# Optimization experiments

Hardware: AMD Instinct MI355X
Metric: run time of the kernel (lower is better)

The kernel has to match this reference:

```python
import jax, jax.numpy as jnp
import numpy as np

V, DW, DH, OUT = 50000, 300, 50, 4
B, T = 1024, 200


def setup_inputs() -> dict:
    key = jax.random.key(0)
    ks = jax.random.split(key, 9)
    x = jax.random.randint(ks[0], (B, T), 0, V)
    lengs = jax.random.randint(ks[1], (B,), 1, T + 1)  # valid lengths >= 1
    k = 1.0 / np.sqrt(DH)
    emb = jax.random.normal(ks[2], (V, DW), jnp.float32)
    emb = emb.at[0].set(0.0)  # padding_idx=0
    w_ih = jax.random.uniform(ks[3], (4 * DH, DW), jnp.float32, -k, k)
    w_hh = jax.random.uniform(ks[4], (4 * DH, DH), jnp.float32, -k, k)
    b_ih = jax.random.uniform(ks[5], (4 * DH,), jnp.float32, -k, k)
    b_hh = jax.random.uniform(ks[6], (4 * DH,), jnp.float32, -k, k)
    w_out = jax.random.uniform(ks[7], (OUT, DH), jnp.float32, -k, k)
    b_out = jax.random.uniform(ks[8], (OUT,), jnp.float32, -k, k)
    return {"x": x, "lengs": lengs, "emb": emb, "w_ih": w_ih, "w_hh": w_hh,
            "b_ih": b_ih, "b_hh": b_hh, "w_out": w_out, "b_out": b_out}


def reference(x, lengs, emb, w_ih, w_hh, b_ih, b_hh, w_out, b_out):
    b, t = x.shape
    xe = emb[x]                                        # [B,T,DW]
    mask = jnp.arange(t)[None, :] < lengs[:, None]     # [B,T] valid steps
    bias = b_ih + b_hh                                 # [4*DH]

    def step(carry, inp):
        h, c = carry
        x_t, m_t = inp                                 # [B,DW], [B]
        g = x_t @ w_ih.T + h @ w_hh.T + bias           # [B,4*DH]
        i, f, gg, o = jnp.split(g, 4, axis=-1)         # torch gate order i,f,g,o
        c_new = jax.nn.sigmoid(f) * c + jax.nn.sigmoid(i) * jnp.tanh(gg)
        h_new = jax.nn.sigmoid(o) * jnp.tanh(c_new)
        m = m_t[:, None]
        # packed-sequence semantics: state frozen past each sequence's length
        return (jnp.where(m, h_new, h), jnp.where(m, c_new, c)), None

    h0 = jnp.zeros((b, DH), xe.dtype)
    (h, _), _ = jax.lax.scan(step, (h0, h0),
                             (xe.transpose(1, 0, 2), mask.T))
    logits = h @ w_out.T + b_out                       # hidden.view(B,-1) -> Linear
    return jax.nn.softmax(logits, axis=1)
```

## Files before the change

kernel.cpp:

```cpp
#include <hip/hip_runtime.h>
#include <math.h>

#define VOCAB 50000
#define DW 300
#define DH 50
#define G4 200
#define BATCH 1024
#define TMAX 200
#define OUTC 4

__global__ __launch_bounds__(256) void transpose_wih(
    const float* __restrict__ w_ih, float* __restrict__ w_T)
{
    int i = blockIdx.x * 256 + threadIdx.x;
    if (i < G4 * DW) {
        int u = i / DW, k = i % DW;
        w_T[k * G4 + u] = w_ih[i];
    }
}

__global__ __launch_bounds__(256, 2) void proj_kernel(
    const float* __restrict__ emb, const float* __restrict__ w_T,
    const float* __restrict__ b_ih, const float* __restrict__ b_hh,
    float* __restrict__ emb_proj)
{
    __shared__ __align__(16) float e_s[100 * 108];
    const int tid = threadIdx.x;
    const int v0 = blockIdx.x * 100;
    const int m_idx = tid / 25;
    const int n_idx = tid % 25;

    float acc[10][8];
#pragma unroll
    for (int m = 0; m < 10; m++)
#pragma unroll
        for (int c = 0; c < 8; c++) acc[m][c] = 0.f;

    for (int kc = 0; kc < DW; kc += 100) {
        __syncthreads();
        for (int i = tid; i < 2500; i += 256) {
            int r = i / 25, c = i % 25;
            float4 v = *(const float4*)&emb[(size_t)(v0 + r) * DW + kc + c * 4];
            *(float4*)&e_s[r * 108 + c * 4] = v;
        }
        __syncthreads();

        if (tid < 250) {
#pragma unroll 2
            for (int kk = 0; kk < 25; kk++) {
                float4 e4[10];
#pragma unroll
                for (int m = 0; m < 10; m++)
                    e4[m] = *(const float4*)&e_s[(m_idx * 10 + m) * 108 + kk * 4];
                const float* wbase = w_T + (size_t)(kc + kk * 4) * G4 + n_idx * 8;
#pragma unroll
                for (int j = 0; j < 4; j++) {
                    float4 wa = *(const float4*)(wbase + j * G4);
                    float4 wb = *(const float4*)(wbase + j * G4 + 4);
#pragma unroll
                    for (int m = 0; m < 10; m++) {
                        float ev = (j == 0) ? e4[m].x : (j == 1) ? e4[m].y
                                 : (j == 2) ? e4[m].z : e4[m].w;
                        acc[m][0] = fmaf(ev, wa.x, acc[m][0]);
                        acc[m][1] = fmaf(ev, wa.y, acc[m][1]);
                        acc[m][2] = fmaf(ev, wa.z, acc[m][2]);
                        acc[m][3] = fmaf(ev, wa.w, acc[m][3]);
                        acc[m][4] = fmaf(ev, wb.x, acc[m][4]);
                        acc[m][5] = fmaf(ev, wb.y, acc[m][5]);
                        acc[m][6] = fmaf(ev, wb.z, acc[m][6]);
                        acc[m][7] = fmaf(ev, wb.w, acc[m][7]);
                    }
                }
            }
        }
    }

    if (tid < 250) {
#pragma unroll
        for (int c = 0; c < 8; c++) {
            int u = n_idx * 8 + c;
            float bias = b_ih[u] + b_hh[u];
            int u2 = (u % DH) * 4 + (u / DH);
#pragma unroll
            for (int m = 0; m < 10; m++)
                emb_proj[(size_t)(v0 + m_idx * 10 + m) * G4 + u2] = acc[m][c] + bias;
        }
    }
}

__device__ __forceinline__ float tanh_f(float x) {
    float e2 = __expf(fminf(2.f * x, 60.f));
    return (e2 - 1.f) / (e2 + 1.f);
}

__global__ __launch_bounds__(64, 1) void lstm_kernel(
    const int* __restrict__ x, const int* __restrict__ lengs,
    const float* __restrict__ emb_proj, const float* __restrict__ w_hh,
    const float* __restrict__ w_out, const float* __restrict__ b_out,
    float* __restrict__ out)
{
    __shared__ __align__(16) float h_s[52];
    __shared__ int x_s[TMAX];
    __shared__ float red[OUTC];

    const int l  = threadIdx.x;
    const int b  = blockIdx.x;
    const int ll = (l < DH) ? l : DH - 1;
    const int len = lengs[b];

    for (int i = l; i < TMAX; i += 64) x_s[i] = x[b * TMAX + i];
    if (l < 52) h_s[l] = 0.f;

    float4 rwi[13], rwf[13], rwg[13], rwo[13];
    {
        const float* wr;
#define LOADROW(dst, gate)                                                    \
        wr = w_hh + (size_t)((gate) * DH + ll) * DH;                          \
        _Pragma("unroll")                                                     \
        for (int k4 = 0; k4 < 12; k4++) {                                     \
            float2 a = *(const float2*)(wr + 4 * k4);                         \
            float2 bb = *(const float2*)(wr + 4 * k4 + 2);                    \
            dst[k4] = make_float4(a.x, a.y, bb.x, bb.y);                      \
        }                                                                     \
        { float2 a = *(const float2*)(wr + 48);                               \
          dst[12] = make_float4(a.x, a.y, 0.f, 0.f); }
        LOADROW(rwi, 0) LOADROW(rwf, 1) LOADROW(rwg, 2) LOADROW(rwo, 3)
#undef LOADROW
    }

    float c_reg = 0.f;
    const float* ep = emb_proj;
    float4 p0 = *(const float4*)(ep + (size_t)x_s[0] * G4 + 4 * ll);
    float4 p1 = *(const float4*)(ep + (size_t)x_s[1 < TMAX ? 1 : 0] * G4 + 4 * ll);

    for (int t = 0; t < len; t++) {
        float4 cur = p0;
        p0 = p1;
        int nt = (t + 2 < TMAX) ? t + 2 : TMAX - 1;
        p1 = *(const float4*)(ep + (size_t)x_s[nt] * G4 + 4 * ll);

        float gi = cur.x, gf = cur.y, gc = cur.z, go = cur.w;
#pragma unroll
        for (int k4 = 0; k4 < 13; k4++) {
            float4 h4 = *(const float4*)&h_s[4 * k4];
            gi = fmaf(h4.x, rwi[k4].x, fmaf(h4.y, rwi[k4].y,
                 fmaf(h4.z, rwi[k4].z, fmaf(h4.w, rwi[k4].w, gi))));
            gf = fmaf(h4.x, rwf[k4].x, fmaf(h4.y, rwf[k4].y,
                 fmaf(h4.z, rwf[k4].z, fmaf(h4.w, rwf[k4].w, gf))));
            gc = fmaf(h4.x, rwg[k4].x, fmaf(h4.y, rwg[k4].y,
                 fmaf(h4.z, rwg[k4].z, fmaf(h4.w, rwg[k4].w, gc))));
            go = fmaf(h4.x, rwo[k4].x, fmaf(h4.y, rwo[k4].y,
                 fmaf(h4.z, rwo[k4].z, fmaf(h4.w, rwo[k4].w, go))));
        }
        float si = 1.f / (1.f + __expf(-gi));
        float sf = 1.f / (1.f + __expf(-gf));
        float so = 1.f / (1.f + __expf(-go));
        float cn = fmaf(sf, c_reg, si * tanh_f(gc));
        c_reg = cn;
        float hn = so * tanh_f(cn);
        if (l < DH) h_s[l] = hn;
    }

    if (l < OUTC) {
        float lg = b_out[l];
        const float* wo = w_out + l * DH;
#pragma unroll
        for (int k = 0; k < DH; k++) lg = fmaf(h_s[k], wo[k], lg);
        red[l] = lg;
    }
    if (l < OUTC) {
        float m = fmaxf(fmaxf(red[0], red[1]), fmaxf(red[2], red[3]));
        float s = 0.f;
#pragma unroll
        for (int j = 0; j < OUTC; j++) s += __expf(red[j] - m);
        out[b * OUTC + l] = __expf(red[l] - m) / s;
    }
}

extern "C" void kernel_launch(void* const* d_in, const int* in_sizes, int n_in,
                              void* d_out, int out_size, void* d_ws, size_t ws_size,
                              hipStream_t stream) {
    const int*   x     = (const int*)d_in[0];
    const int*   lengs = (const int*)d_in[1];
    const float* emb   = (const float*)d_in[2];
    const float* w_ih  = (const float*)d_in[3];
    const float* w_hh  = (const float*)d_in[4];
    const float* b_ih  = (const float*)d_in[5];
    const float* b_hh  = (const float*)d_in[6];
    const float* w_out = (const float*)d_in[7];
    const float* b_out = (const float*)d_in[8];
    float* out = (float*)d_out;

    float* emb_proj = (float*)d_ws;
    float* w_T      = emb_proj + (size_t)VOCAB * G4;

    hipLaunchKernelGGL(transpose_wih, dim3((G4 * DW + 255) / 256), dim3(256),
                       0, stream, w_ih, w_T);
    hipLaunchKernelGGL(proj_kernel, dim3(VOCAB / 100), dim3(256), 0, stream,
                       emb, w_T, b_ih, b_hh, emb_proj);
    hipLaunchKernelGGL(lstm_kernel, dim3(BATCH), dim3(64), 0, stream,
                       x, lengs, emb_proj, w_hh, w_out, b_out, out);
}
```

Measured before the change: 351.4 us.

## Split LSTM gate work across two lanes per hidden unit with DPP exchange

```diff
diff --git a/kernel.cpp b/kernel.cpp
--- a/kernel.cpp
+++ b/kernel.cpp
@@ -88,92 +88,116 @@
     }
 }
 
-__device__ __forceinline__ float tanh_f(float x) {
-    float e2 = __expf(fminf(2.f * x, 60.f));
-    return (e2 - 1.f) / (e2 + 1.f);
-}
-
-__global__ __launch_bounds__(64, 1) void lstm_kernel(
+__device__ __forceinline__ float dpp_xor1(float x) {
+    return __int_as_float(__builtin_amdgcn_update_dpp(
+        0, __float_as_int(x), 0xB1, 0xF, 0xF, true));
+}
+
+__global__ __launch_bounds__(128, 2) void lstm_kernel(
     const int* __restrict__ x, const int* __restrict__ lengs,
     const float* __restrict__ emb_proj, const float* __restrict__ w_hh,
     const float* __restrict__ w_out, const float* __restrict__ b_out,
     float* __restrict__ out)
 {
-    __shared__ __align__(16) float h_s[52];
+    __shared__ __align__(16) float hbuf[2][52];
     __shared__ int x_s[TMAX];
     __shared__ float red[OUTC];
 
-    const int l  = threadIdx.x;
-    const int b  = blockIdx.x;
-    const int ll = (l < DH) ? l : DH - 1;
+    const int tid = threadIdx.x;
+    const int b   = blockIdx.x;
+    const int u   = tid >> 1;
+    const int uu  = (u < DH) ? u : 0;
+    const int odd = tid & 1;
     const int len = lengs[b];
 
-    for (int i = l; i < TMAX; i += 64) x_s[i] = x[b * TMAX + i];
-    if (l < 52) h_s[l] = 0.f;
-
-    float4 rwi[13], rwf[13], rwg[13], rwo[13];
+    for (int i = tid; i < TMAX; i += 128) x_s[i] = x[b * TMAX + i];
+    if (tid < 52) hbuf[0][tid] = 0.f;
+
+    float wA[DH], wB[DH];
     {
-        const float* wr;
-#define LOADROW(dst, gate)                                                    \
-        wr = w_hh + (size_t)((gate) * DH + ll) * DH;                          \
-        _Pragma("unroll")                                                     \
-        for (int k4 = 0; k4 < 12; k4++) {                                     \
-            float2 a = *(const float2*)(wr + 4 * k4);                         \
-            float2 bb = *(const float2*)(wr + 4 * k4 + 2);                    \
-            dst[k4] = make_float4(a.x, a.y, bb.x, bb.y);                      \
-        }                                                                     \
-        { float2 a = *(const float2*)(wr + 48);                               \
-          dst[12] = make_float4(a.x, a.y, 0.f, 0.f); }
-        LOADROW(rwi, 0) LOADROW(rwf, 1) LOADROW(rwg, 2) LOADROW(rwo, 3)
-#undef LOADROW
-    }
-
+        const float* rA = w_hh + (size_t)((2 * odd) * DH + uu) * DH;
+        const float* rB = w_hh + (size_t)((2 * odd + 1) * DH + uu) * DH;
+#pragma unroll
+        for (int k = 0; k < 25; k++) {
+            float2 a  = *(const float2*)(rA + 2 * k);
+            float2 bb = *(const float2*)(rB + 2 * k);
+            wA[2 * k] = a.x;  wA[2 * k + 1] = a.y;
+            wB[2 * k] = bb.x; wB[2 * k + 1] = bb.y;
+        }
+    }
+    __syncthreads();
+
+    const int col = (u < DH) ? (tid * 2) : 0;
+    const float* ep = emb_proj;
+    float2 p0 = *(const float2*)(ep + (size_t)x_s[0] * G4 + col);
+    float2 p1 = *(const float2*)(ep + (size_t)x_s[1] * G4 + col);
+    float2 p2 = *(const float2*)(ep + (size_t)x_s[2] * G4 + col);
     float c_reg = 0.f;
-    const float* ep = emb_proj;
-    float4 p0 = *(const float4*)(ep + (size_t)x_s[0] * G4 + 4 * ll);
-    float4 p1 = *(const float4*)(ep + (size_t)x_s[1 < TMAX ? 1 : 0] * G4 + 4 * ll);
 
     for (int t = 0; t < len; t++) {
-        float4 cur = p0;
-        p0 = p1;
-        int nt = (t + 2 < TMAX) ? t + 2 : TMAX - 1;
-        p1 = *(const float4*)(ep + (size_t)x_s[nt] * G4 + 4 * ll);
-
-        float gi = cur.x, gf = cur.y, gc = cur.z, go = cur.w;
-#pragma unroll
-        for (int k4 = 0; k4 < 13; k4++) {
-            float4 h4 = *(const float4*)&h_s[4 * k4];
-            gi = fmaf(h4.x, rwi[k4].x, fmaf(h4.y, rwi[k4].y,
-                 fmaf(h4.z, rwi[k4].z, fmaf(h4.w, rwi[k4].w, gi))));
-            gf = fmaf(h4.x, rwf[k4].x, fmaf(h4.y, rwf[k4].y,
-                 fmaf(h4.z, rwf[k4].z, fmaf(h4.w, rwf[k4].w, gf))));
-            gc = fmaf(h4.x, rwg[k4].x, fmaf(h4.y, rwg[k4].y,
-                 fmaf(h4.z, rwg[k4].z, fmaf(h4.w, rwg[k4].w, gc))));
-            go = fmaf(h4.x, rwo[k4].x, fmaf(h4.y, rwo[k4].y,
-                 fmaf(h4.z, rwo[k4].z, fmaf(h4.w, rwo[k4].w, go))));
-        }
-        float si = 1.f / (1.f + __expf(-gi));
-        float sf = 1.f / (1.f + __expf(-gf));
-        float so = 1.f / (1.f + __expf(-go));
-        float cn = fmaf(sf, c_reg, si * tanh_f(gc));
+        float2 cur = p0; p0 = p1; p1 = p2;
+        int nt = t + 3; nt = (nt < TMAX) ? nt : TMAX - 1;
+        p2 = *(const float2*)(ep + (size_t)x_s[nt] * G4 + col);
+
+        const float* hb = hbuf[t & 1];
+        float accA0 = 0.f, accA1 = 0.f, accB0 = 0.f, accB1 = 0.f;
+#pragma unroll
+        for (int k4 = 0; k4 < 12; k4++) {
+            float4 h4 = *(const float4*)(hb + 4 * k4);
+            if ((k4 & 1) == 0) {
+                accA0 = fmaf(h4.x, wA[4*k4], fmaf(h4.y, wA[4*k4+1],
+                        fmaf(h4.z, wA[4*k4+2], fmaf(h4.w, wA[4*k4+3], accA0))));
+                accB0 = fmaf(h4.x, wB[4*k4], fmaf(h4.y, wB[4*k4+1],
+                        fmaf(h4.z, wB[4*k4+2], fmaf(h4.w, wB[4*k4+3], accB0))));
+            } else {
+                accA1 = fmaf(h4.x, wA[4*k4], fmaf(h4.y, wA[4*k4+1],
+                        fmaf(h4.z, wA[4*k4+2], fmaf(h4.w, wA[4*k4+3], accA1))));
+                accB1 = fmaf(h4.x, wB[4*k4], fmaf(h4.y, wB[4*k4+1],
+                        fmaf(h4.z, wB[4*k4+2], fmaf(h4.w, wB[4*k4+3], accB1))));
+            }
+        }
+        {
+            float2 h2 = *(const float2*)(hb + 48);
+            accA0 = fmaf(h2.x, wA[48], fmaf(h2.y, wA[49], accA0));
+            accB1 = fmaf(h2.x, wB[48], fmaf(h2.y, wB[49], accB1));
+        }
+        float gA = cur.x + accA0 + accA1;
+        float gB = cur.y + accB0 + accB1;
+
+        float yA = odd ? 2.f * gA : gA;
+        float sA = 1.f / (1.f + __expf(-yA));
+        float vA = odd ? fmaf(2.f, sA, -1.f) : sA;
+        float vB = 1.f / (1.f + __expf(-gB));
+
+        float oA = dpp_xor1(vA);
+        float oB = dpp_xor1(vB);
+        float si = odd ? oA : vA;
+        float sf = odd ? oB : vB;
+        float tg = odd ? vA : oA;
+        float so = odd ? vB : oB;
+
+        float cn = fmaf(sf, c_reg, si * tg);
         c_reg = cn;
-        float hn = so * tanh_f(cn);
-        if (l < DH) h_s[l] = hn;
-    }
-
-    if (l < OUTC) {
-        float lg = b_out[l];
-        const float* wo = w_out + l * DH;
-#pragma unroll
-        for (int k = 0; k < DH; k++) lg = fmaf(h_s[k], wo[k], lg);
-        red[l] = lg;
-    }
-    if (l < OUTC) {
+        float th = fmaf(2.f, 1.f / (1.f + __expf(-2.f * cn)), -1.f);
+        float hn = so * th;
+        if (!odd && u < DH) hbuf[(t + 1) & 1][u] = hn;
+        __syncthreads();
+    }
+
+    const float* hf = hbuf[len & 1];
+    if (tid < OUTC) {
+        float lg = b_out[tid];
+        const float* wo = w_out + tid * DH;
+#pragma unroll
+        for (int k = 0; k < DH; k++) lg = fmaf(hf[k], wo[k], lg);
+        red[tid] = lg;
+    }
+    if (tid < OUTC) {
         float m = fmaxf(fmaxf(red[0], red[1]), fmaxf(red[2], red[3]));
         float s = 0.f;
 #pragma unroll
         for (int j = 0; j < OUTC; j++) s += __expf(red[j] - m);
-        out[b * OUTC + l] = __expf(red[l] - m) / s;
+        out[b * OUTC + tid] = __expf(red[tid] - m) / s;
     }
 }
 
@@ -198,6 +222,6 @@
                        0, stream, w_ih, w_T);
     hipLaunchKernelGGL(proj_kernel, dim3(VOCAB / 100), dim3(256), 0, stream,
                        emb, w_T, b_ih, b_hh, emb_proj);
-    hipLaunchKernelGGL(lstm_kernel, dim3(BATCH), dim3(64), 0, stream,
+    hipLaunchKernelGGL(lstm_kernel, dim3(BATCH), dim3(128), 0, stream,
                        x, lengs, emb_proj, w_hh, w_out, b_out, out);
 }
```

New measurement: 330.9 us. 1.06x faster.

## Permute gate columns in transposed weights, prefetch weights, vectorize projection stores

Applied to the files above, without the earlier changes.

```diff
diff --git a/kernel.cpp b/kernel.cpp
--- a/kernel.cpp
+++ b/kernel.cpp
@@ -15,7 +15,8 @@
     int i = blockIdx.x * 256 + threadIdx.x;
     if (i < G4 * DW) {
         int u = i / DW, k = i % DW;
-        w_T[k * G4 + u] = w_ih[i];
+        int u2 = (u % DH) * 4 + (u / DH);
+        w_T[k * G4 + u2] = w_ih[i];
     }
 }
 
@@ -36,6 +37,8 @@
 #pragma unroll
         for (int c = 0; c < 8; c++) acc[m][c] = 0.f;
 
+    const float* wcol = w_T + n_idx * 8;
+
     for (int kc = 0; kc < DW; kc += 100) {
         __syncthreads();
         for (int i = tid; i < 2500; i += 256) {
@@ -46,44 +49,63 @@
         __syncthreads();
 
         if (tid < 250) {
-#pragma unroll 2
+            float4 wa[4], wb[4];
+#pragma unroll
+            for (int j = 0; j < 4; j++) {
+                const float* p = wcol + (size_t)(kc + j) * G4;
+                wa[j] = *(const float4*)p;
+                wb[j] = *(const float4*)(p + 4);
+            }
             for (int kk = 0; kk < 25; kk++) {
+                float4 na[4], nb[4];
+                int kn = kc + ((kk < 24) ? (kk + 1) : kk) * 4;
+#pragma unroll
+                for (int j = 0; j < 4; j++) {
+                    const float* p = wcol + (size_t)(kn + j) * G4;
+                    na[j] = *(const float4*)p;
+                    nb[j] = *(const float4*)(p + 4);
+                }
                 float4 e4[10];
 #pragma unroll
                 for (int m = 0; m < 10; m++)
                     e4[m] = *(const float4*)&e_s[(m_idx * 10 + m) * 108 + kk * 4];
-                const float* wbase = w_T + (size_t)(kc + kk * 4) * G4 + n_idx * 8;
 #pragma unroll
                 for (int j = 0; j < 4; j++) {
-                    float4 wa = *(const float4*)(wbase + j * G4);
-                    float4 wb = *(const float4*)(wbase + j * G4 + 4);
 #pragma unroll
                     for (int m = 0; m < 10; m++) {
                         float ev = (j == 0) ? e4[m].x : (j == 1) ? e4[m].y
                                  : (j == 2) ? e4[m].z : e4[m].w;
-                        acc[m][0] = fmaf(ev, wa.x, acc[m][0]);
-                        acc[m][1] = fmaf(ev, wa.y, acc[m][1]);
-                        acc[m][2] = fmaf(ev, wa.z, acc[m][2]);
-                        acc[m][3] = fmaf(ev, wa.w, acc[m][3]);
-                        acc[m][4] = fmaf(ev, wb.x, acc[m][4]);
-                        acc[m][5] = fmaf(ev, wb.y, acc[m][5]);
-                        acc[m][6] = fmaf(ev, wb.z, acc[m][6]);
-                        acc[m][7] = fmaf(ev, wb.w, acc[m][7]);
+                        acc[m][0] = fmaf(ev, wa[j].x, acc[m][0]);
+                        acc[m][1] = fmaf(ev, wa[j].y, acc[m][1]);
+                        acc[m][2] = fmaf(ev, wa[j].z, acc[m][2]);
+                        acc[m][3] = fmaf(ev, wa[j].w, acc[m][3]);
+                        acc[m][4] = fmaf(ev, wb[j].x, acc[m][4]);
+                        acc[m][5] = fmaf(ev, wb[j].y, acc[m][5]);
+                        acc[m][6] = fmaf(ev, wb[j].z, acc[m][6]);
+                        acc[m][7] = fmaf(ev, wb[j].w, acc[m][7]);
                     }
                 }
+#pragma unroll
+                for (int j = 0; j < 4; j++) { wa[j] = na[j]; wb[j] = nb[j]; }
             }
         }
     }
 
     if (tid < 250) {
+        float bias[8];
 #pragma unroll
         for (int c = 0; c < 8; c++) {
-            int u = n_idx * 8 + c;
-            float bias = b_ih[u] + b_hh[u];
-            int u2 = (u % DH) * 4 + (u / DH);
-#pragma unroll
-            for (int m = 0; m < 10; m++)
-                emb_proj[(size_t)(v0 + m_idx * 10 + m) * G4 + u2] = acc[m][c] + bias;
+            int u2 = n_idx * 8 + c;
+            int u  = (u2 & 3) * DH + (u2 >> 2);
+            bias[c] = b_ih[u] + b_hh[u];
+        }
+#pragma unroll
+        for (int m = 0; m < 10; m++) {
+            float* dst = &emb_proj[(size_t)(v0 + m_idx * 10 + m) * G4 + n_idx * 8];
+            *(float4*)dst = make_float4(acc[m][0] + bias[0], acc[m][1] + bias[1],
+                                        acc[m][2] + bias[2], acc[m][3] + bias[3]);
+            *(float4*)(dst + 4) = make_float4(acc[m][4] + bias[4], acc[m][5] + bias[5],
+                                              acc[m][6] + bias[6], acc[m][7] + bias[7]);
         }
     }
 }
@@ -93,7 +115,9 @@
     return (e2 - 1.f) / (e2 + 1.f);
 }
 
-__global__ __launch_bounds__(64, 1) void lstm_kernel(
+__global__ __launch_bounds__(64)
+__attribute__((amdgpu_waves_per_eu(1, 1)))
+void lstm_kernel(
     const int* __restrict__ x, const int* __restrict__ lengs,
     const float* __restrict__ emb_proj, const float* __restrict__ w_hh,
     const float* __restrict__ w_out, const float* __restrict__ b_out,
@@ -131,7 +155,7 @@
     float c_reg = 0.f;
     const float* ep = emb_proj;
     float4 p0 = *(const float4*)(ep + (size_t)x_s[0] * G4 + 4 * ll);
-    float4 p1 = *(const float4*)(ep + (size_t)x_s[1 < TMAX ? 1 : 0] * G4 + 4 * ll);
+    float4 p1 = *(const float4*)(ep + (size_t)x_s[1] * G4 + 4 * ll);
 
     for (int t = 0; t < len; t++) {
         float4 cur = p0;
```

After: 325.7 us. 1.08x faster.
